# Optimization experiments

Measured on AMD Instinct MI355X. Metric: run time of the kernel, lower is better.

The kernel has to match this reference:

```python
import jax, jax.numpy as jnp
import numpy as np


def setup_inputs() -> dict:
    key = jax.random.key(0)
    k1, _ = jax.random.split(key)
    B, S, D = 4, 4096, 64
    inp = jax.random.normal(k1, (B, S, D), dtype=jnp.float32)
    attn_mask = jnp.zeros((S, S), dtype=bool)  # no masked positions
    return {"input": inp, "attn_mask": attn_mask}


def reference(input, attn_mask):
    # attn_mask: bool [S,S] -> additive mask with -inf at masked positions
    am = jnp.where(attn_mask, -jnp.inf, 0.0).T  # transpose(0,1)
    # scores: [B,S,S]
    v = jnp.einsum('bsd,btd->bst', input, input)
    mask = (1.0 - am) * -10000.0
    v = v + mask  # dead in original module too: w is drawn fresh below
    # w = empty_like(v).uniform_(-0.1, 0.1)
    wkey = jax.random.key(42)
    w = jax.random.uniform(wkey, v.shape, dtype=v.dtype, minval=-0.1, maxval=0.1)
    w = jax.nn.softmax(w, axis=-1)
    # per-column (dim 1) L1 renorm: w[:, i] /= ||w[:, i]||_1 over (batch, last dim)
    denom = jnp.sum(jnp.abs(w), axis=(0, 2), keepdims=True)  # [1,S,1]
    w = w / denom
    return jnp.einsum('bst,btd->bsd', w, input)
```

## Files before the change

kernel.cpp:

```cpp
#include <hip/hip_runtime.h>
#include <hip/hip_bf16.h>
#include <stdint.h>


#define S_ 4096
#define D_ 64

typedef __attribute__((ext_vector_type(8))) short short8v;
typedef __attribute__((ext_vector_type(4))) float floatx4;

__device__ __forceinline__ uint32_t rotl32(uint32_t x, unsigned r) {
    return (x << r) | (x >> (32u - r));
}

__device__ __forceinline__ uint32_t threefry_bits(uint32_t f) {
    const uint32_t k0 = 0u, k1 = 42u;
    const uint32_t k2 = 0x1BD11BDAu ^ k0 ^ k1;
    uint32_t x0 = k0;
    uint32_t x1 = f + k1;
#define TFR(r) { x0 += x1; x1 = rotl32(x1, (r)); x1 ^= x0; }
    TFR(13) TFR(15) TFR(26) TFR(6)
    x0 += k1; x1 += k2 + 1u;
    TFR(17) TFR(29) TFR(16) TFR(24)
    x0 += k2; x1 += k0 + 2u;
    TFR(13) TFR(15) TFR(26) TFR(6)
    x0 += k0; x1 += k1 + 3u;
    TFR(17) TFR(29) TFR(16) TFR(24)
    x0 += k1; x1 += k2 + 4u;
    TFR(13) TFR(15) TFR(26) TFR(6)
    x0 += k2; x1 += k0 + 5u;
#undef TFR
    return x0 ^ x1;
}

__device__ __forceinline__ float uniform_exp_poly(uint32_t bits) {
    const float t = __uint_as_float((bits >> 9) | 0x3F800000u);
    const float u = __builtin_fmaf(t, 0.2f, -0.3f);
    float p = __builtin_fmaf(u, 0.16666667f, 0.5f);
    p = __builtin_fmaf(p, u, 1.0f);
    return __builtin_fmaf(p, u, 1.0f);
}

__device__ __forceinline__ uint32_t cvt_pk_bf16(float e0, float e1) {
    uint32_t r;
    asm("v_cvt_pk_bf16_f32 %0, %1, %2" : "=v"(r) : "v"(e0), "v"(e1));
    return r;
}

__device__ __forceinline__ short8v gen_a(uint32_t c0, float& zpA, float& zpB) {
    union { uint32_t u[4]; short8v v; } a;
#pragma unroll
    for (int jp = 0; jp < 4; ++jp) {
        const float e0 = uniform_exp_poly(threefry_bits(c0 + 2u * jp));
        const float e1 = uniform_exp_poly(threefry_bits(c0 + 2u * jp + 1u));
        zpA += e0;
        zpB += e1;
        a.u[jp] = cvt_pk_bf16(e0, e1);
    }
    return a.v;
}

__global__ __launch_bounds__(64) void pack_xt_bf16(
    const float* __restrict__ x, short* __restrict__ bf)
{
    const int id = blockIdx.x;
    const int l  = threadIdx.x;
    const int kc = id & 127;
    const int dg = (id >> 7) & 3;
    const int b  = id >> 9;
    const int d  = dg * 16 + (l & 15);
    const int k0 = kc * 32 + (l >> 4) * 8;
    const float* __restrict__ xb = x + (size_t)b * (S_ * D_);
    union { short8v v; short s[8]; } r;
#pragma unroll
    for (int j = 0; j < 8; ++j) {
        __hip_bfloat16 h = __float2bfloat16(xb[(size_t)(k0 + j) * D_ + d]);
        r.s[j] = __builtin_bit_cast(short, h);
    }
    *(short8v*)&bf[(size_t)id * 512 + l * 8] = r.v;
}

__global__ __launch_bounds__(512, 6) void fused_rand_attn_mfma3(
    const short* __restrict__ bf, float* __restrict__ out)
{
    const int tid  = threadIdx.x;
    const int bid  = (blockIdx.x & 7) * 128 + (blockIdx.x >> 3);
    const int b    = bid >> 8;
    const int s0   = (bid & 255) * 16;
    const int w    = tid >> 6;
    const int lane = tid & 63;
    const int lt   = lane & 15;
    const int lh   = lane >> 4;

    __shared__ float ACC[8][4][64][4];
    __shared__ float ZL[8][16];

    floatx4 acc0 = {0.f,0.f,0.f,0.f}, acc1 = {0.f,0.f,0.f,0.f};
    floatx4 acc2 = {0.f,0.f,0.f,0.f}, acc3 = {0.f,0.f,0.f,0.f};
    float zpA = 0.f, zpB = 0.f;

    const short* __restrict__ bl =
        bf + (size_t)b * (4 * 128 * 512) + (size_t)lane * 8;
    const uint32_t fl = (((uint32_t)b << 24) | ((uint32_t)(s0 + lt) << 12))
                        + (uint32_t)(lh * 8);

#pragma unroll 1
    for (int kt = w; kt < 64; kt += 8) {
        const short* pk = bl + (size_t)kt * 1024;
        const uint32_t kb = fl + ((uint32_t)kt << 6);

        const short8v b00 = *(const short8v*)(pk);
        const short8v b10 = *(const short8v*)(pk + 65536);
        const short8v b20 = *(const short8v*)(pk + 131072);
        const short8v b30 = *(const short8v*)(pk + 196608);

        const short8v a0 = gen_a(kb, zpA, zpB);

        const short8v b01 = *(const short8v*)(pk + 512);
        const short8v b11 = *(const short8v*)(pk + 65536 + 512);
        const short8v b21 = *(const short8v*)(pk + 131072 + 512);
        const short8v b31 = *(const short8v*)(pk + 196608 + 512);

        acc0 = __builtin_amdgcn_mfma_f32_16x16x32_bf16(a0, b00, acc0, 0, 0, 0);
        acc1 = __builtin_amdgcn_mfma_f32_16x16x32_bf16(a0, b10, acc1, 0, 0, 0);
        acc2 = __builtin_amdgcn_mfma_f32_16x16x32_bf16(a0, b20, acc2, 0, 0, 0);
        acc3 = __builtin_amdgcn_mfma_f32_16x16x32_bf16(a0, b30, acc3, 0, 0, 0);

        const short8v a1 = gen_a(kb + 32u, zpA, zpB);

        acc0 = __builtin_amdgcn_mfma_f32_16x16x32_bf16(a1, b01, acc0, 0, 0, 0);
        acc1 = __builtin_amdgcn_mfma_f32_16x16x32_bf16(a1, b11, acc1, 0, 0, 0);
        acc2 = __builtin_amdgcn_mfma_f32_16x16x32_bf16(a1, b21, acc2, 0, 0, 0);
        acc3 = __builtin_amdgcn_mfma_f32_16x16x32_bf16(a1, b31, acc3, 0, 0, 0);
    }

    float zp = zpA + zpB;
    zp += __shfl_xor(zp, 16);
    zp += __shfl_xor(zp, 32);
    if (lane < 16) ZL[w][lane] = zp;
    *(floatx4*)&ACC[w][0][lane][0] = acc0;
    *(floatx4*)&ACC[w][1][lane][0] = acc1;
    *(floatx4*)&ACC[w][2][lane][0] = acc2;
    *(floatx4*)&ACC[w][3][lane][0] = acc3;
    __syncthreads();

    const int dg = w & 3;
    const int rh = w >> 2;
    floatx4 facc = {0.f,0.f,0.f,0.f};
#pragma unroll
    for (int w2 = 0; w2 < 8; ++w2) {
        const floatx4 t = *(const floatx4*)&ACC[w2][dg][lane][0];
        facc.x += t.x; facc.y += t.y; facc.z += t.z; facc.w += t.w;
    }
    const float v0 = rh ? facc.z : facc.x;
    const float v1 = rh ? facc.w : facc.y;
    const int row0 = lh * 4 + rh * 2;
    float Z0 = 0.f, Z1 = 0.f;
#pragma unroll
    for (int w2 = 0; w2 < 8; ++w2) {
        Z0 += ZL[w2][row0];
        Z1 += ZL[w2][row0 + 1];
    }
    const int col = dg * 16 + lt;
    out[((size_t)b * S_ + (s0 + row0)) * D_ + col]     = v0 * (0.25f / Z0);
    out[((size_t)b * S_ + (s0 + row0 + 1)) * D_ + col] = v1 * (0.25f / Z1);
}

extern "C" void kernel_launch(void* const* d_in, const int* in_sizes, int n_in,
                              void* d_out, int out_size, void* d_ws, size_t ws_size,
                              hipStream_t stream) {
    const float* x = (const float*)d_in[0];
    float* out = (float*)d_out;
    short* bfw = (short*)d_ws;
    (void)in_sizes; (void)n_in; (void)out_size; (void)ws_size;
    hipLaunchKernelGGL(pack_xt_bf16, dim3(2048), dim3(64), 0, stream, x, bfw);
    hipLaunchKernelGGL(fused_rand_attn_mfma3, dim3(1024), dim3(512), 0, stream,
                       bfw, out);
}
```

Measured before the change: 133.2 us.

## Use hardware exp2, interleave paired threefry streams, and relayout packed keys

Replaces the cubic polynomial exp approximation with a single fma plus hardware exp2 on the raw mantissa bits, which is closer to exact softmax. Threefry is computed for two counters at once with rotate builtins to expose ILP. The packed bf16 key buffer is reordered so each k-tile's eight B fragments are contiguous (4KB per tile) instead of strided by 128KB. Occupancy hint raised from 6 to 8 waves per EU. These aim to cut VALU cost of RNG and exp and to improve B-fragment locality, at the risk of register pressure under the tighter launch bound.

```diff
diff --git a/kernel.cpp b/kernel.cpp
--- a/kernel.cpp
+++ b/kernel.cpp
@@ -6,39 +6,40 @@
 #define S_ 4096
 #define D_ 64
 
+#define EXP_A ((float)(0.2 * 1.4426950408889634 / 8388608.0))
+#define EXP_B ((float)(-0.1 * 1.4426950408889634))
+
 typedef __attribute__((ext_vector_type(8))) short short8v;
 typedef __attribute__((ext_vector_type(4))) float floatx4;
 
-__device__ __forceinline__ uint32_t rotl32(uint32_t x, unsigned r) {
-    return (x << r) | (x >> (32u - r));
+__device__ __forceinline__ void tf2(uint32_t f0, uint32_t f1,
+                                    uint32_t& r0, uint32_t& r1) {
+    const uint32_t k1 = 42u, k2 = 0x1BD11BDAu ^ 42u;
+    uint32_t a0 = 0u,      b0 = f0 + k1;
+    uint32_t a1 = 0u,      b1 = f1 + k1;
+#define R2(r) { a0 += b0; a1 += b1;                         \
+                b0 = __builtin_rotateleft32(b0, (r));       \
+                b1 = __builtin_rotateleft32(b1, (r));       \
+                b0 ^= a0; b1 ^= a1; }
+    R2(13) R2(15) R2(26) R2(6)
+    a0 += k1; b0 += k2 + 1u;   a1 += k1; b1 += k2 + 1u;
+    R2(17) R2(29) R2(16) R2(24)
+    a0 += k2; b0 += 2u;        a1 += k2; b1 += 2u;
+    R2(13) R2(15) R2(26) R2(6)
+    b0 += k1 + 3u;             b1 += k1 + 3u;
+    R2(17) R2(29) R2(16) R2(24)
+    a0 += k1; b0 += k2 + 4u;   a1 += k1; b1 += k2 + 4u;
+    R2(13) R2(15) R2(26) R2(6)
+    a0 += k2; b0 += 5u;        a1 += k2; b1 += 5u;
+#undef R2
+    r0 = a0 ^ b0;
+    r1 = a1 ^ b1;
 }
 
-__device__ __forceinline__ uint32_t threefry_bits(uint32_t f) {
-    const uint32_t k0 = 0u, k1 = 42u;
-    const uint32_t k2 = 0x1BD11BDAu ^ k0 ^ k1;
-    uint32_t x0 = k0;
-    uint32_t x1 = f + k1;
-#define TFR(r) { x0 += x1; x1 = rotl32(x1, (r)); x1 ^= x0; }
-    TFR(13) TFR(15) TFR(26) TFR(6)
-    x0 += k1; x1 += k2 + 1u;
-    TFR(17) TFR(29) TFR(16) TFR(24)
-    x0 += k2; x1 += k0 + 2u;
-    TFR(13) TFR(15) TFR(26) TFR(6)
-    x0 += k0; x1 += k1 + 3u;
-    TFR(17) TFR(29) TFR(16) TFR(24)
-    x0 += k1; x1 += k2 + 4u;
-    TFR(13) TFR(15) TFR(26) TFR(6)
-    x0 += k2; x1 += k0 + 5u;
-#undef TFR
-    return x0 ^ x1;
-}
-
-__device__ __forceinline__ float uniform_exp_poly(uint32_t bits) {
-    const float t = __uint_as_float((bits >> 9) | 0x3F800000u);
-    const float u = __builtin_fmaf(t, 0.2f, -0.3f);
-    float p = __builtin_fmaf(u, 0.16666667f, 0.5f);
-    p = __builtin_fmaf(p, u, 1.0f);
-    return __builtin_fmaf(p, u, 1.0f);
+__device__ __forceinline__ float uexp(uint32_t bits) {
+    const float fm = (float)(bits >> 9);
+    const float arg = __builtin_fmaf(fm, EXP_A, EXP_B);
+    return __builtin_amdgcn_exp2f(arg);
 }
 
 __device__ __forceinline__ uint32_t cvt_pk_bf16(float e0, float e1) {
@@ -47,14 +48,16 @@
     return r;
 }
 
-__device__ __forceinline__ short8v gen_a(uint32_t c0, float& zpA, float& zpB) {
+__device__ __forceinline__ short8v gen_a(uint32_t c0, float& zp0, float& zp1) {
     union { uint32_t u[4]; short8v v; } a;
 #pragma unroll
     for (int jp = 0; jp < 4; ++jp) {
-        const float e0 = uniform_exp_poly(threefry_bits(c0 + 2u * jp));
-        const float e1 = uniform_exp_poly(threefry_bits(c0 + 2u * jp + 1u));
-        zpA += e0;
-        zpB += e1;
+        uint32_t r0, r1;
+        tf2(c0 + 2u * jp, c0 + 2u * jp + 1u, r0, r1);
+        const float e0 = uexp(r0);
+        const float e1 = uexp(r1);
+        zp0 += e0;
+        zp1 += e1;
         a.u[jp] = cvt_pk_bf16(e0, e1);
     }
     return a.v;
@@ -65,11 +68,12 @@
 {
     const int id = blockIdx.x;
     const int l  = threadIdx.x;
-    const int kc = id & 127;
-    const int dg = (id >> 7) & 3;
+    const int dg = id & 3;
+    const int kc = (id >> 2) & 1;
+    const int kt = (id >> 3) & 63;
     const int b  = id >> 9;
     const int d  = dg * 16 + (l & 15);
-    const int k0 = kc * 32 + (l >> 4) * 8;
+    const int k0 = kt * 64 + kc * 32 + (l >> 4) * 8;
     const float* __restrict__ xb = x + (size_t)b * (S_ * D_);
     union { short8v v; short s[8]; } r;
 #pragma unroll
@@ -80,7 +84,7 @@
     *(short8v*)&bf[(size_t)id * 512 + l * 8] = r.v;
 }
 
-__global__ __launch_bounds__(512, 6) void fused_rand_attn_mfma3(
+__global__ __launch_bounds__(512, 8) void fused_rand_attn_mfma4(
     const short* __restrict__ bf, float* __restrict__ out)
 {
     const int tid  = threadIdx.x;
@@ -100,26 +104,26 @@
     float zpA = 0.f, zpB = 0.f;
 
     const short* __restrict__ bl =
-        bf + (size_t)b * (4 * 128 * 512) + (size_t)lane * 8;
+        bf + (size_t)b * (64 * 4096) + (size_t)lane * 8;
     const uint32_t fl = (((uint32_t)b << 24) | ((uint32_t)(s0 + lt) << 12))
                         + (uint32_t)(lh * 8);
 
 #pragma unroll 1
     for (int kt = w; kt < 64; kt += 8) {
-        const short* pk = bl + (size_t)kt * 1024;
+        const short* pk = bl + (size_t)kt * 4096;
         const uint32_t kb = fl + ((uint32_t)kt << 6);
 
         const short8v b00 = *(const short8v*)(pk);
-        const short8v b10 = *(const short8v*)(pk + 65536);
-        const short8v b20 = *(const short8v*)(pk + 131072);
-        const short8v b30 = *(const short8v*)(pk + 196608);
+        const short8v b10 = *(const short8v*)(pk + 512);
+        const short8v b20 = *(const short8v*)(pk + 1024);
+        const short8v b30 = *(const short8v*)(pk + 1536);
 
         const short8v a0 = gen_a(kb, zpA, zpB);
 
-        const short8v b01 = *(const short8v*)(pk + 512);
-        const short8v b11 = *(const short8v*)(pk + 65536 + 512);
-        const short8v b21 = *(const short8v*)(pk + 131072 + 512);
-        const short8v b31 = *(const short8v*)(pk + 196608 + 512);
+        const short8v b01 = *(const short8v*)(pk + 2048);
+        const short8v b11 = *(const short8v*)(pk + 2560);
+        const short8v b21 = *(const short8v*)(pk + 3072);
+        const short8v b31 = *(const short8v*)(pk + 3584);
 
         acc0 = __builtin_amdgcn_mfma_f32_16x16x32_bf16(a0, b00, acc0, 0, 0, 0);
         acc1 = __builtin_amdgcn_mfma_f32_16x16x32_bf16(a0, b10, acc1, 0, 0, 0);
@@ -174,6 +178,6 @@
     short* bfw = (short*)d_ws;
     (void)in_sizes; (void)n_in; (void)out_size; (void)ws_size;
     hipLaunchKernelGGL(pack_xt_bf16, dim3(2048), dim3(64), 0, stream, x, bfw);
-    hipLaunchKernelGGL(fused_rand_attn_mfma3, dim3(1024), dim3(512), 0, stream,
+    hipLaunchKernelGGL(fused_rand_attn_mfma4, dim3(1024), dim3(512), 0, stream,
                        bfw, out);
 }
```

Result: no change. 135.8 us (+1.9%).
